# Kernel tuning notes

Measured on AMD Instinct MI355X. Metric: run time of the kernel, lower is better.

## Reference

```python
import jax, jax.numpy as jnp
import numpy as np

B, C, T = 2048, 8, 1024
EPS = 1e-5
SLOPE = 1.0 / 128.0


def leaky(x):
    # F.leaky_relu(x, 1/128)
    return jnp.where(x >= 0, x, SLOPE * x)


def batchnorm(h, g, b):
    # training-mode BatchNorm1d over [B, C, T]: stats over (batch, time), biased var
    m = h.mean(axis=(0, 2), keepdims=True)
    v = jnp.mean((h - m) ** 2, axis=(0, 2), keepdims=True)
    return (h - m) * jax.lax.rsqrt(v + EPS) * g[None, :, None] + b[None, :, None]


def setup_inputs() -> dict:
    key = jax.random.key(0)
    ks = jax.random.split(key, 8)
    x = jax.random.normal(ks[0], (B, C, T), dtype=jnp.float32)
    # reservoir pushforward: low-bit random matrix scaled to spectral radius 0.1
    A_raw = jax.random.normal(ks[1], (C, C), dtype=jnp.float32)
    rho = jnp.max(jnp.abs(np.linalg.eigvals(np.asarray(A_raw))))
    A = (0.1 * A_raw / rho).astype(jnp.float32)
    w1 = jax.random.normal(ks[2], (24, 8), dtype=jnp.float32) * (1.0 / np.sqrt(8))
    b1 = jax.random.normal(ks[3], (24,), dtype=jnp.float32) * 0.01
    w2 = jax.random.normal(ks[4], (16, 24), dtype=jnp.float32) * (1.0 / np.sqrt(24))
    b2 = jax.random.normal(ks[5], (16,), dtype=jnp.float32) * 0.01
    w3 = jax.random.normal(ks[6], (11, 48), dtype=jnp.float32) * (1.0 / np.sqrt(48))
    b3 = jax.random.normal(ks[7], (11,), dtype=jnp.float32) * 0.01
    return {
        "x": x, "A": A,
        "bn1_g": jnp.ones((8,), jnp.float32), "bn1_b": jnp.zeros((8,), jnp.float32),
        "w1": w1, "b1": b1, "w2": w2, "b2": b2, "w3": w3, "b3": b3,
        "bn2_g": jnp.ones((11,), jnp.float32), "bn2_b": jnp.zeros((11,), jnp.float32),
    }


def reference(x, A, bn1_g, bn1_b, w1, b1, w2, b2, w3, b3, bn2_g, bn2_b):
    bw = batchnorm(x, bn1_g, bn1_b)  # [B,8,T]

    # --- FSDDRC reservoir: 1024-step sequential recurrence on 8-dim state ---
    xs = jnp.transpose(bw, (2, 0, 1))  # [T,B,8]

    def step(f, xt):
        # nonlin(A @ f + x_t) with nonlin(z) = clamp(4z, -1, 1)
        f_new = jnp.clip(4.0 * (f @ A.T + xt), -1.0, 1.0)
        return f_new, jnp.concatenate([f_new, leaky(f_new)], axis=-1)  # [B,16]

    f0 = jnp.zeros_like(xs[0])
    _, outs = jax.lax.scan(step, f0, xs)  # [T,B,16]
    nl_tdyn = jnp.transpose(outs, (1, 2, 0))  # [B,16,T]

    # --- feedforward branch (mtmt = linear over channel dim) ---
    h = leaky(jnp.einsum("bct,oc->bot", bw, w1) + b1[None, :, None])  # [B,24,T]
    ff = leaky(jnp.einsum("bct,oc->bot", h, w2) + b2[None, :, None])  # [B,16,T]

    stacked = jnp.concatenate([x, bw, ff, nl_tdyn], axis=1)  # [B,48,T]
    pre = jnp.einsum("bct,oc->bot", stacked, w3) + b3[None, :, None]  # [B,11,T]
    assimilated = leaky(batchnorm(pre, bn2_g, bn2_b))
    return assimilated.mean(axis=-1)  # [B,11]
```

## Files before the change

### kernel.cpp

```cpp
#include <hip/hip_runtime.h>
#include <hip/hip_fp16.h>

#define NB 2048
#define NC 8
#define NT 1024
#define EPS 1e-5f
#define SLOPE (1.0f/128.0f)
#define NELEM (2048.0f*1024.0f)
#define TB (NT*NB)

#define PAR_OFF 9216
#define PF_S4  0
#define PF_O4  8
#define PF_B1F 16
#define PF_B2F 40
#define PF_B3F 56
#define PU_A4   96
#define PU_W1   128
#define PU_W2   224
#define PU_W3X  416
#define PU_W3F  460
#define PU_W3L  504
#define PU_W3FF 548
#define XT_BYTE  65536
#define PWS_BYTE (65536 + 2048*1024*8*2)

typedef _Float16 h2 __attribute__((ext_vector_type(2)));
typedef __fp16  fp16v2 __attribute__((ext_vector_type(2)));
union U32H2 { unsigned u; h2 h; fp16v2 f; unsigned short us[2]; };

__device__ __forceinline__ float leaky(float z){ return fmaxf(z, z*SLOPE); }
__device__ __forceinline__ unsigned short f2h(float v){ return __half_as_ushort(__float2half(v)); }
__device__ __forceinline__ float h2f(unsigned short u){ return __half2float(__ushort_as_half(u)); }
__device__ __forceinline__ h2 uph2(unsigned u){ U32H2 x; x.u = u; return x.h; }
__device__ __forceinline__ h2 pk(float a, float b){
    U32H2 x; x.f = __builtin_amdgcn_cvt_pkrtz(a, b); return x.h;
}

#if defined(__has_builtin)
#if __has_builtin(__builtin_amdgcn_fdot2)
#define HAVE_FDOT2 1
#endif
#endif
#ifdef HAVE_FDOT2
__device__ __forceinline__ float fdot2(h2 a, h2 b, float c){ return __builtin_amdgcn_fdot2(a, b, c, false); }
#else
__device__ __forceinline__ float fdot2(h2 a, h2 b, float c){
    return c + (float)a[0]*(float)b[0] + (float)a[1]*(float)b[1];
}
#endif

__global__ __launch_bounds__(256) void k0_tr(const float* __restrict__ x,
                                             unsigned short* __restrict__ xT,
                                             float* __restrict__ ws)
{
    __shared__ unsigned short tile[64*134];
    __shared__ float sred[4][4][2];
    const int tid = threadIdx.x;
    const int bg = blockIdx.x >> 4;
    const int tg = blockIdx.x & 15;
    const int b0 = bg*16, t0 = tg*64;
    float s = 0.f, s2 = 0.f;
#pragma unroll
    for(int r=0;r<8;r++){
        const int flat4 = r*256 + tid;
        const int row = flat4 >> 4;
        const int t4  = flat4 & 15;
        const int b = row >> 3, c = row & 7;
        float4 v = *(const float4*)(x + (size_t)(b0+b)*8192 + c*1024 + t0 + t4*4);
        s  += v.x+v.y+v.z+v.w;
        s2 += v.x*v.x+v.y*v.y+v.z*v.z+v.w*v.w;
        const int base = b*8 + c;
        tile[(t4*4+0)*134 + base] = f2h(v.x);
        tile[(t4*4+1)*134 + base] = f2h(v.y);
        tile[(t4*4+2)*134 + base] = f2h(v.z);
        tile[(t4*4+3)*134 + base] = f2h(v.w);
    }
#pragma unroll
    for(int m=8;m>=1;m>>=1){ s += __shfl_xor(s,m,64); s2 += __shfl_xor(s2,m,64); }
    const int lane = tid & 63, wave = tid >> 6;
    if((lane & 15) == 0){ sred[wave][lane>>4][0] = s; sred[wave][lane>>4][1] = s2; }
    __syncthreads();
    if(tid < 16){
        const int c = tid & 7, which = tid >> 3;
        const int w0 = (c < 4) ? 0 : 1, g = c & 3;
        const float v = sred[w0][g][which] + sred[w0+2][g][which];
        atomicAdd(&ws[(blockIdx.x & 63)*16 + which*8 + c], v);
    }
#pragma unroll
    for(int r=0;r<8;r++){
        const int q = r*256 + tid;
        const int t = q >> 5, inner = q & 31;
        const unsigned int lo = *(const unsigned int*)&tile[t*134 + inner*4];
        const unsigned int hi = *(const unsigned int*)&tile[t*134 + inner*4 + 2];
        *(uint2*)(xT + ((size_t)(t0+t)*NB + b0)*8 + inner*4) = make_uint2(lo, hi);
    }
}

__device__ __forceinline__ unsigned pk2u(float a, float b){
    U32H2 v; v.us[0] = f2h(a); v.us[1] = f2h(b); return v.u;
}
__global__ __launch_bounds__(256) void k2_fold(const float* __restrict__ g1, const float* __restrict__ bb1,
    const float* __restrict__ w1, const float* __restrict__ b1,
    const float* __restrict__ w2, const float* __restrict__ b2,
    const float* __restrict__ w3, const float* __restrict__ b3,
    const float* __restrict__ A, float* __restrict__ ws)
{
    float* par = ws + PAR_OFF;
    unsigned* paru = (unsigned*)par;
    __shared__ float st[16];
    __shared__ float sc[8], oc[8];
    const int tid = threadIdx.x;
    if(tid<16){
        float s=0.f;
        for(int i=0;i<64;i++) s += ws[i*16+tid];
        st[tid]=s;
    }
    __syncthreads();
    if(tid<8){
        const float inv = 1.0f/NELEM;
        float m  = st[tid]*inv;
        float v  = st[8+tid]*inv - m*m;
        float s_ = g1[tid]*rsqrtf(v+EPS);
        float o_ = bb1[tid] - m*s_;
        sc[tid]=s_; oc[tid]=o_;
        par[PF_S4+tid]=4.f*s_; par[PF_O4+tid]=4.f*o_;
    }
    __syncthreads();
    if(tid<24){ float a=b1[tid]; for(int c=0;c<8;c++) a += w1[tid*8+c]*oc[c]; par[PF_B1F+tid]=a; }
    if(tid<16){ par[PF_B2F+tid]=b2[tid]; }
    if(tid<11){ float a=b3[tid]; for(int c=0;c<8;c++) a += w3[tid*48+8+c]*oc[c]; par[PF_B3F+tid]=a; }
    if(tid<96){ int o=tid>>2, j=tid&3;
        paru[PU_W1+tid] = pk2u(w1[o*8+2*j]*sc[2*j], w1[o*8+2*j+1]*sc[2*j+1]); }
    if(tid<192){ int o=tid/12, j=tid-o*12;
        paru[PU_W2+tid] = pk2u(w2[o*24+2*j], w2[o*24+2*j+1]); }
    if(tid<44){ int o=tid>>2, j=tid&3; int c0=2*j, c1=2*j+1;
        float xa = w3[o*48+c0] + w3[o*48+8+c0]*sc[c0];
        float xb = w3[o*48+c1] + w3[o*48+8+c1]*sc[c1];
        paru[PU_W3X+tid] = pk2u(xa, xb);
        paru[PU_W3F+tid] = pk2u(w3[o*48+32+c0], w3[o*48+32+c1]);
        paru[PU_W3L+tid] = pk2u(w3[o*48+40+c0], w3[o*48+40+c1]);
    }
    if(tid<88){ int o=tid>>3, j=tid&7;
        paru[PU_W3FF+tid] = pk2u(w3[o*48+16+2*j], w3[o*48+16+2*j+1]); }
    if(tid<32){ int i=tid>>2, j=tid&3;
        paru[PU_A4+tid] = pk2u(4.f*A[i*8+2*j], 4.f*A[i*8+2*j+1]); }
}

__global__ __launch_bounds__(256,8) void k34(
    const unsigned short* __restrict__ xT,
    float* __restrict__ ws, unsigned short* __restrict__ pws)
{
    const float* par = ws + PAR_OFF;
    const unsigned* pu = (const unsigned*)par;
    const int tid = threadIdx.x;
    const int b  = (blockIdx.x >> 8)*256 + tid;
    const int tg = blockIdx.x & 255;
    const int t0 = tg*4;
    const int tw = (t0 >= 16) ? (t0 - 16) : 0;
    const int tend = t0 + 4;

    h2 fh[4];
#pragma unroll
    for(int j=0;j<4;j++) fh[j] = pk(0.f, 0.f);
    float s1[11], s2[11];
#pragma unroll
    for(int o=0;o<11;o++){ s1[o]=0.f; s2[o]=0.f; }

    for(int t=tw; t<tend; t++){
        union { float4 v; unsigned u[4]; unsigned short us[8]; } ux;
        ux.v = *(const float4*)(xT + ((size_t)t*NB + b)*8);
        h2 xh[4];
#pragma unroll
        for(int j=0;j<4;j++) xh[j] = uph2(ux.u[j]);
        float nf[8];
#pragma unroll
        for(int i=0;i<8;i++){
            float acc = fmaf(par[PF_S4+i], h2f(ux.us[i]), par[PF_O4+i]);
#pragma unroll
            for(int j=0;j<4;j++) acc = fdot2(uph2(pu[PU_A4+i*4+j]), fh[j], acc);
            nf[i] = fminf(fmaxf(acc,-1.f),1.f);
        }
#pragma unroll
        for(int j=0;j<4;j++) fh[j] = pk(nf[2*j], nf[2*j+1]);
        if(t >= t0){
            h2 lfh[4];
#pragma unroll
            for(int j=0;j<4;j++) lfh[j] = pk(leaky(nf[2*j]), leaky(nf[2*j+1]));
            h2 hh[12];
#pragma unroll
            for(int p=0;p<12;p++){
                float za = par[PF_B1F+2*p], zb = par[PF_B1F+2*p+1];
#pragma unroll
                for(int j=0;j<4;j++){
                    za = fdot2(uph2(pu[PU_W1+(2*p)*4+j]),   xh[j], za);
                    zb = fdot2(uph2(pu[PU_W1+(2*p+1)*4+j]), xh[j], zb);
                }
                hh[p] = pk(leaky(za), leaky(zb));
            }
            h2 ffh[8];
#pragma unroll
            for(int p=0;p<8;p++){
                float za = par[PF_B2F+2*p], zb = par[PF_B2F+2*p+1];
#pragma unroll
                for(int j=0;j<12;j++){
                    za = fdot2(uph2(pu[PU_W2+(2*p)*12+j]),   hh[j], za);
                    zb = fdot2(uph2(pu[PU_W2+(2*p+1)*12+j]), hh[j], zb);
                }
                ffh[p] = pk(leaky(za), leaky(zb));
            }
            const size_t base = (size_t)t*NB + b;
#pragma unroll
            for(int o=0;o<11;o++){
                float z = par[PF_B3F+o];
#pragma unroll
                for(int j=0;j<4;j++) z = fdot2(uph2(pu[PU_W3X+o*4+j]),  xh[j],  z);
#pragma unroll
                for(int j=0;j<4;j++) z = fdot2(uph2(pu[PU_W3F+o*4+j]),  fh[j],  z);
#pragma unroll
                for(int j=0;j<4;j++) z = fdot2(uph2(pu[PU_W3L+o*4+j]),  lfh[j], z);
#pragma unroll
                for(int j=0;j<8;j++) z = fdot2(uph2(pu[PU_W3FF+o*8+j]), ffh[j], z);
                s1[o] += z; s2[o] += z*z;
                pws[(size_t)o*TB + base] = f2h(z);
            }
        }
    }
#pragma unroll
    for(int o=0;o<11;o++){
#pragma unroll
        for(int m=32;m>=1;m>>=1){ s1[o]+=__shfl_xor(s1[o],m,64); s2[o]+=__shfl_xor(s2[o],m,64); }
    }
    __shared__ float red[4][22];
    const int wave=tid>>6, lane=tid&63;
    if(lane==0){
#pragma unroll
        for(int o=0;o<11;o++){ red[wave][o]=s1[o]; red[wave][11+o]=s2[o]; }
    }
    __syncthreads();
    if(tid<22){
        float tot = red[0][tid]+red[1][tid]+red[2][tid]+red[3][tid];
        atomicAdd(&ws[1024 + (blockIdx.x & 255)*32 + tid], tot);
    }
}

__global__ __launch_bounds__(256) void k6(const float* __restrict__ g2, const float* __restrict__ bb2,
                                          const float* __restrict__ ws,
                                          const unsigned short* __restrict__ pws,
                                          float* __restrict__ out)
{
    const int o  = blockIdx.x >> 5;
    const int r  = blockIdx.x & 31;
    const int bg = r & 1, tg = r >> 1;
    const int tid = threadIdx.x;

    __shared__ float red[4][2];
    __shared__ float sal, sbe;
    {
        float p1 = ws[1024 + tid*32 + o];
        float p2 = ws[1024 + tid*32 + 11 + o];
#pragma unroll
        for(int m=32;m>=1;m>>=1){ p1 += __shfl_xor(p1,m,64); p2 += __shfl_xor(p2,m,64); }
        const int wave = tid>>6, lane = tid&63;
        if(lane==0){ red[wave][0]=p1; red[wave][1]=p2; }
        __syncthreads();
        if(tid==0){
            float t1 = red[0][0]+red[1][0]+red[2][0]+red[3][0];
            float t2 = red[0][1]+red[1][1]+red[2][1]+red[3][1];
            const float inv = 1.0f/NELEM;
            float m = t1*inv;
            float v = t2*inv - m*m;
            float a = g2[o]*rsqrtf(v+EPS);
            sal = a; sbe = bb2[o] - m*a;
        }
        __syncthreads();
    }
    const float al = sal, be = sbe;

    const int b0 = bg*1024 + tid*4;
    const unsigned short* pp = pws + (size_t)o*TB + b0;
    float acc0=0.f, acc1=0.f, acc2=0.f, acc3=0.f;
#pragma unroll 8
    for(int i=0;i<64;i++){
        const int t = tg*64 + i;
        uint2 u = *(const uint2*)(pp + (size_t)t*NB);
        U32H2 ua, ub; ua.u = u.x; ub.u = u.y;
        acc0 += leaky(fmaf(al, h2f(ua.us[0]), be));
        acc1 += leaky(fmaf(al, h2f(ua.us[1]), be));
        acc2 += leaky(fmaf(al, h2f(ub.us[0]), be));
        acc3 += leaky(fmaf(al, h2f(ub.us[1]), be));
    }
    atomicAdd(&out[(b0+0)*11+o], acc0*(1.0f/NT));
    atomicAdd(&out[(b0+1)*11+o], acc1*(1.0f/NT));
    atomicAdd(&out[(b0+2)*11+o], acc2*(1.0f/NT));
    atomicAdd(&out[(b0+3)*11+o], acc3*(1.0f/NT));
}

extern "C" void kernel_launch(void* const* d_in, const int* in_sizes, int n_in,
                              void* d_out, int out_size, void* d_ws, size_t ws_size,
                              hipStream_t stream)
{
    const float* x   = (const float*)d_in[0];
    const float* A   = (const float*)d_in[1];
    const float* g1  = (const float*)d_in[2];
    const float* bb1 = (const float*)d_in[3];
    const float* w1  = (const float*)d_in[4];
    const float* b1  = (const float*)d_in[5];
    const float* w2  = (const float*)d_in[6];
    const float* b2  = (const float*)d_in[7];
    const float* w3  = (const float*)d_in[8];
    const float* b3  = (const float*)d_in[9];
    const float* g2  = (const float*)d_in[10];
    const float* bb2 = (const float*)d_in[11];
    float* out = (float*)d_out;
    float* ws  = (float*)d_ws;
    unsigned short* xT  = (unsigned short*)((char*)d_ws + XT_BYTE);
    unsigned short* pws = (unsigned short*)((char*)d_ws + PWS_BYTE);

    (void)hipMemsetAsync(d_ws, 0, 40960, stream);
    (void)hipMemsetAsync(d_out, 0, (size_t)out_size*4, stream);
    k0_tr  <<<2048, 256, 0, stream>>>(x, xT, ws);
    k2_fold<<<1,    256, 0, stream>>>(g1, bb1, w1, b1, w2, b2, w3, b3, A, ws);
    k34    <<<2048, 256, 0, stream>>>(xT, ws, pws);
    k6     <<<352,  256, 0, stream>>>(g2, bb2, ws, pws, out);
}
```

Before: 249.4 us.

## Double time chunk per block and process timestep pairs sharing weight loads

Each k34 block now covers 8 timesteps instead of 4, so the 16-step recurrence warmup is amortised over twice as many outputs and half as many blocks are launched. The output phase handles two timesteps at once, so each packed weight loaded from the parameter area feeds two dot products. Leaky-ReLU now runs on packed halves and the clamp uses a single med3 instruction. The trade-off is more live registers, which is why the launch bound drops to 4 waves, and fewer, longer blocks with less parallelism.

```diff
diff --git a/kernel.cpp b/kernel.cpp
--- a/kernel.cpp
+++ b/kernel.cpp
@@ -36,6 +36,11 @@
 __device__ __forceinline__ h2 pk(float a, float b){
     U32H2 x; x.f = __builtin_amdgcn_cvt_pkrtz(a, b); return x.h;
 }
+__device__ __forceinline__ h2 leaky2(h2 v){
+    h2 s = v * (_Float16)SLOPE;
+    return __builtin_elementwise_max(v, s);
+}
+__device__ __forceinline__ float clamp1(float z){ return __builtin_amdgcn_fmed3f(z, -1.f, 1.f); }
 
 #if defined(__has_builtin)
 #if __has_builtin(__builtin_amdgcn_fdot2)
@@ -147,18 +152,17 @@
         paru[PU_A4+tid] = pk2u(4.f*A[i*8+2*j], 4.f*A[i*8+2*j+1]); }
 }
 
-__global__ __launch_bounds__(256,8) void k34(
+__global__ __launch_bounds__(256,4) void k34(
     const unsigned short* __restrict__ xT,
     float* __restrict__ ws, unsigned short* __restrict__ pws)
 {
     const float* par = ws + PAR_OFF;
     const unsigned* pu = (const unsigned*)par;
     const int tid = threadIdx.x;
-    const int b  = (blockIdx.x >> 8)*256 + tid;
-    const int tg = blockIdx.x & 255;
-    const int t0 = tg*4;
+    const int b  = (blockIdx.x >> 7)*256 + tid;
+    const int tg = blockIdx.x & 127;
+    const int t0 = tg*8;
     const int tw = (t0 >= 16) ? (t0 - 16) : 0;
-    const int tend = t0 + 4;
 
     h2 fh[4];
 #pragma unroll
@@ -167,63 +171,109 @@
 #pragma unroll
     for(int o=0;o<11;o++){ s1[o]=0.f; s2[o]=0.f; }
 
-    for(int t=tw; t<tend; t++){
+    for(int t=tw; t<t0; t++){
         union { float4 v; unsigned u[4]; unsigned short us[8]; } ux;
         ux.v = *(const float4*)(xT + ((size_t)t*NB + b)*8);
-        h2 xh[4];
-#pragma unroll
-        for(int j=0;j<4;j++) xh[j] = uph2(ux.u[j]);
         float nf[8];
 #pragma unroll
         for(int i=0;i<8;i++){
             float acc = fmaf(par[PF_S4+i], h2f(ux.us[i]), par[PF_O4+i]);
 #pragma unroll
             for(int j=0;j<4;j++) acc = fdot2(uph2(pu[PU_A4+i*4+j]), fh[j], acc);
-            nf[i] = fminf(fmaxf(acc,-1.f),1.f);
+            nf[i] = clamp1(acc);
         }
 #pragma unroll
         for(int j=0;j<4;j++) fh[j] = pk(nf[2*j], nf[2*j+1]);
-        if(t >= t0){
-            h2 lfh[4];
-#pragma unroll
-            for(int j=0;j<4;j++) lfh[j] = pk(leaky(nf[2*j]), leaky(nf[2*j+1]));
-            h2 hh[12];
-#pragma unroll
-            for(int p=0;p<12;p++){
-                float za = par[PF_B1F+2*p], zb = par[PF_B1F+2*p+1];
-#pragma unroll
-                for(int j=0;j<4;j++){
-                    za = fdot2(uph2(pu[PU_W1+(2*p)*4+j]),   xh[j], za);
-                    zb = fdot2(uph2(pu[PU_W1+(2*p+1)*4+j]), xh[j], zb);
-                }
-                hh[p] = pk(leaky(za), leaky(zb));
-            }
-            h2 ffh[8];
-#pragma unroll
-            for(int p=0;p<8;p++){
-                float za = par[PF_B2F+2*p], zb = par[PF_B2F+2*p+1];
-#pragma unroll
-                for(int j=0;j<12;j++){
-                    za = fdot2(uph2(pu[PU_W2+(2*p)*12+j]),   hh[j], za);
-                    zb = fdot2(uph2(pu[PU_W2+(2*p+1)*12+j]), hh[j], zb);
-                }
-                ffh[p] = pk(leaky(za), leaky(zb));
-            }
-            const size_t base = (size_t)t*NB + b;
-#pragma unroll
-            for(int o=0;o<11;o++){
-                float z = par[PF_B3F+o];
-#pragma unroll
-                for(int j=0;j<4;j++) z = fdot2(uph2(pu[PU_W3X+o*4+j]),  xh[j],  z);
-#pragma unroll
-                for(int j=0;j<4;j++) z = fdot2(uph2(pu[PU_W3F+o*4+j]),  fh[j],  z);
-#pragma unroll
-                for(int j=0;j<4;j++) z = fdot2(uph2(pu[PU_W3L+o*4+j]),  lfh[j], z);
-#pragma unroll
-                for(int j=0;j<8;j++) z = fdot2(uph2(pu[PU_W3FF+o*8+j]), ffh[j], z);
-                s1[o] += z; s2[o] += z*z;
-                pws[(size_t)o*TB + base] = f2h(z);
-            }
+    }
+
+    for(int tp=0; tp<4; tp++){
+        const int t = t0 + tp*2;
+        h2 xh2[2][4], fh2[2][4];
+#pragma unroll
+        for(int u=0;u<2;u++){
+            union { float4 v; unsigned uu[4]; unsigned short us[8]; } ux;
+            ux.v = *(const float4*)(xT + ((size_t)(t+u)*NB + b)*8);
+#pragma unroll
+            for(int j=0;j<4;j++) xh2[u][j] = uph2(ux.uu[j]);
+            float nf[8];
+#pragma unroll
+            for(int i=0;i<8;i++){
+                float acc = fmaf(par[PF_S4+i], h2f(ux.us[i]), par[PF_O4+i]);
+#pragma unroll
+                for(int j=0;j<4;j++) acc = fdot2(uph2(pu[PU_A4+i*4+j]), fh[j], acc);
+                nf[i] = clamp1(acc);
+            }
+#pragma unroll
+            for(int j=0;j<4;j++){ fh[j] = pk(nf[2*j], nf[2*j+1]); fh2[u][j] = fh[j]; }
+        }
+        h2 hh2[2][12];
+#pragma unroll
+        for(int p=0;p<12;p++){
+            float za0 = par[PF_B1F+2*p], zb0 = par[PF_B1F+2*p+1];
+            float za1 = za0, zb1 = zb0;
+#pragma unroll
+            for(int j=0;j<4;j++){
+                h2 wa = uph2(pu[PU_W1+(2*p)*4+j]);
+                h2 wb = uph2(pu[PU_W1+(2*p+1)*4+j]);
+                za0 = fdot2(wa, xh2[0][j], za0);
+                za1 = fdot2(wa, xh2[1][j], za1);
+                zb0 = fdot2(wb, xh2[0][j], zb0);
+                zb1 = fdot2(wb, xh2[1][j], zb1);
+            }
+            hh2[0][p] = leaky2(pk(za0, zb0));
+            hh2[1][p] = leaky2(pk(za1, zb1));
+        }
+        h2 ff2[2][8];
+#pragma unroll
+        for(int p=0;p<8;p++){
+            float za0 = par[PF_B2F+2*p], zb0 = par[PF_B2F+2*p+1];
+            float za1 = za0, zb1 = zb0;
+#pragma unroll
+            for(int j=0;j<12;j++){
+                h2 wa = uph2(pu[PU_W2+(2*p)*12+j]);
+                h2 wb = uph2(pu[PU_W2+(2*p+1)*12+j]);
+                za0 = fdot2(wa, hh2[0][j], za0);
+                za1 = fdot2(wa, hh2[1][j], za1);
+                zb0 = fdot2(wb, hh2[0][j], zb0);
+                zb1 = fdot2(wb, hh2[1][j], zb1);
+            }
+            ff2[0][p] = leaky2(pk(za0, zb0));
+            ff2[1][p] = leaky2(pk(za1, zb1));
+        }
+        h2 lf2[2][4];
+#pragma unroll
+        for(int u=0;u<2;u++)
+#pragma unroll
+            for(int j=0;j<4;j++) lf2[u][j] = leaky2(fh2[u][j]);
+        const size_t base = (size_t)t*NB + b;
+#pragma unroll
+        for(int o=0;o<11;o++){
+            float z0 = par[PF_B3F+o], z1 = z0;
+#pragma unroll
+            for(int j=0;j<4;j++){
+                h2 w = uph2(pu[PU_W3X+o*4+j]);
+                z0 = fdot2(w, xh2[0][j], z0); z1 = fdot2(w, xh2[1][j], z1);
+            }
+#pragma unroll
+            for(int j=0;j<4;j++){
+                h2 w = uph2(pu[PU_W3F+o*4+j]);
+                z0 = fdot2(w, fh2[0][j], z0); z1 = fdot2(w, fh2[1][j], z1);
+            }
+#pragma unroll
+            for(int j=0;j<4;j++){
+                h2 w = uph2(pu[PU_W3L+o*4+j]);
+                z0 = fdot2(w, lf2[0][j], z0); z1 = fdot2(w, lf2[1][j], z1);
+            }
+#pragma unroll
+            for(int j=0;j<8;j++){
+                h2 w = uph2(pu[PU_W3FF+o*8+j]);
+                z0 = fdot2(w, ff2[0][j], z0); z1 = fdot2(w, ff2[1][j], z1);
+            }
+            s1[o] += z0 + z1;
+            s2[o] = fmaf(z0, z0, s2[o]);
+            s2[o] = fmaf(z1, z1, s2[o]);
+            pws[(size_t)o*TB + base]      = f2h(z0);
+            pws[(size_t)o*TB + base + NB] = f2h(z1);
         }
     }
 #pragma unroll
@@ -321,6 +371,6 @@
     (void)hipMemsetAsync(d_out, 0, (size_t)out_size*4, stream);
     k0_tr  <<<2048, 256, 0, stream>>>(x, xT, ws);
     k2_fold<<<1,    256, 0, stream>>>(g1, bb1, w1, b1, w2, b2, w3, b3, A, ws);
-    k34    <<<2048, 256, 0, stream>>>(xT, ws, pws);
+    k34    <<<1024, 256, 0, stream>>>(xT, ws, pws);
     k6     <<<352,  256, 0, stream>>>(g2, bb2, ws, pws, out);
 }
```

New measurement: 229.1 us. 8.1% less time.

## Switch recurrence and MLP to fp32 FMA with 8-step time tiles

Applied to the files above, without the earlier changes.

Replaces the packed fp16 fdot2 arithmetic in the fused reservoir/MLP kernel with plain fp32 FMAs on fp32 parameters. Each block now covers 8 time steps instead of 4, so the 16-step warm-up recurrence is amortised over twice as many outputs, and the block count is halved. Occupancy hint drops from 8 to 4, clamping uses fmed3, and zeroing of the output moves into the fold kernel, removing a memset. The fp32 path roughly doubles the arithmetic instructions per output compared with dot2 and raises register pressure.

```diff
diff --git a/kernel.cpp b/kernel.cpp
--- a/kernel.cpp
+++ b/kernel.cpp
@@ -10,45 +10,25 @@
 #define TB (NT*NB)
 
 #define PAR_OFF 9216
-#define PF_S4  0
-#define PF_O4  8
-#define PF_B1F 16
-#define PF_B2F 40
-#define PF_B3F 56
-#define PU_A4   96
-#define PU_W1   128
-#define PU_W2   224
-#define PU_W3X  416
-#define PU_W3F  460
-#define PU_W3L  504
-#define PU_W3FF 548
+#define PF_S4    0
+#define PF_O4    8
+#define PF_B1F   16
+#define PF_B2F   40
+#define PF_B3F   56
+#define PF_A4F   128
+#define PF_W1F   192
+#define PF_W2F   384
+#define PF_W3XF  768
+#define PF_W3FP  856
+#define PF_W3LP  944
+#define PF_W3FFP 1032
 #define XT_BYTE  65536
 #define PWS_BYTE (65536 + 2048*1024*8*2)
-
-typedef _Float16 h2 __attribute__((ext_vector_type(2)));
-typedef __fp16  fp16v2 __attribute__((ext_vector_type(2)));
-union U32H2 { unsigned u; h2 h; fp16v2 f; unsigned short us[2]; };
 
 __device__ __forceinline__ float leaky(float z){ return fmaxf(z, z*SLOPE); }
 __device__ __forceinline__ unsigned short f2h(float v){ return __half_as_ushort(__float2half(v)); }
 __device__ __forceinline__ float h2f(unsigned short u){ return __half2float(__ushort_as_half(u)); }
-__device__ __forceinline__ h2 uph2(unsigned u){ U32H2 x; x.u = u; return x.h; }
-__device__ __forceinline__ h2 pk(float a, float b){
-    U32H2 x; x.f = __builtin_amdgcn_cvt_pkrtz(a, b); return x.h;
-}
-
-#if defined(__has_builtin)
-#if __has_builtin(__builtin_amdgcn_fdot2)
-#define HAVE_FDOT2 1
-#endif
-#endif
-#ifdef HAVE_FDOT2
-__device__ __forceinline__ float fdot2(h2 a, h2 b, float c){ return __builtin_amdgcn_fdot2(a, b, c, false); }
-#else
-__device__ __forceinline__ float fdot2(h2 a, h2 b, float c){
-    return c + (float)a[0]*(float)b[0] + (float)a[1]*(float)b[1];
-}
-#endif
+__device__ __forceinline__ float clamp1(float z){ return __builtin_amdgcn_fmed3f(z, -1.f, 1.f); }
 
 __global__ __launch_bounds__(256) void k0_tr(const float* __restrict__ x,
                                              unsigned short* __restrict__ xT,
@@ -97,17 +77,14 @@
     }
 }
 
-__device__ __forceinline__ unsigned pk2u(float a, float b){
-    U32H2 v; v.us[0] = f2h(a); v.us[1] = f2h(b); return v.u;
-}
 __global__ __launch_bounds__(256) void k2_fold(const float* __restrict__ g1, const float* __restrict__ bb1,
     const float* __restrict__ w1, const float* __restrict__ b1,
     const float* __restrict__ w2, const float* __restrict__ b2,
     const float* __restrict__ w3, const float* __restrict__ b3,
-    const float* __restrict__ A, float* __restrict__ ws)
+    const float* __restrict__ A, float* __restrict__ ws,
+    float* __restrict__ out)
 {
     float* par = ws + PAR_OFF;
-    unsigned* paru = (unsigned*)par;
     __shared__ float st[16];
     __shared__ float sc[8], oc[8];
     const int tid = threadIdx.x;
@@ -130,100 +107,107 @@
     if(tid<24){ float a=b1[tid]; for(int c=0;c<8;c++) a += w1[tid*8+c]*oc[c]; par[PF_B1F+tid]=a; }
     if(tid<16){ par[PF_B2F+tid]=b2[tid]; }
     if(tid<11){ float a=b3[tid]; for(int c=0;c<8;c++) a += w3[tid*48+8+c]*oc[c]; par[PF_B3F+tid]=a; }
-    if(tid<96){ int o=tid>>2, j=tid&3;
-        paru[PU_W1+tid] = pk2u(w1[o*8+2*j]*sc[2*j], w1[o*8+2*j+1]*sc[2*j+1]); }
-    if(tid<192){ int o=tid/12, j=tid-o*12;
-        paru[PU_W2+tid] = pk2u(w2[o*24+2*j], w2[o*24+2*j+1]); }
-    if(tid<44){ int o=tid>>2, j=tid&3; int c0=2*j, c1=2*j+1;
-        float xa = w3[o*48+c0] + w3[o*48+8+c0]*sc[c0];
-        float xb = w3[o*48+c1] + w3[o*48+8+c1]*sc[c1];
-        paru[PU_W3X+tid] = pk2u(xa, xb);
-        paru[PU_W3F+tid] = pk2u(w3[o*48+32+c0], w3[o*48+32+c1]);
-        paru[PU_W3L+tid] = pk2u(w3[o*48+40+c0], w3[o*48+40+c1]);
-    }
-    if(tid<88){ int o=tid>>3, j=tid&7;
-        paru[PU_W3FF+tid] = pk2u(w3[o*48+16+2*j], w3[o*48+16+2*j+1]); }
-    if(tid<32){ int i=tid>>2, j=tid&3;
-        paru[PU_A4+tid] = pk2u(4.f*A[i*8+2*j], 4.f*A[i*8+2*j+1]); }
-}
-
-__global__ __launch_bounds__(256,8) void k34(
+    if(tid<64){ par[PF_A4F+tid] = 4.f*A[tid]; }
+    if(tid<192){ const int c = tid & 7; par[PF_W1F+tid] = w1[tid]*sc[c]; }
+    for(int i=tid;i<384;i+=256) par[PF_W2F+i] = w2[i];
+    if(tid<88){
+        const int o = tid >> 3, c = tid & 7;
+        par[PF_W3XF+tid] = w3[o*48+c] + w3[o*48+8+c]*sc[c];
+        par[PF_W3FP+tid] = w3[o*48+32+c];
+        par[PF_W3LP+tid] = w3[o*48+40+c];
+    }
+    if(tid<176){ const int o = tid >> 4, c = tid & 15; par[PF_W3FFP+tid] = w3[o*48+16+c]; }
+    for(int i=tid;i<2048*11;i+=256) out[i] = 0.f;
+}
+
+__global__ __launch_bounds__(256,4) void k34(
     const unsigned short* __restrict__ xT,
     float* __restrict__ ws, unsigned short* __restrict__ pws)
 {
     const float* par = ws + PAR_OFF;
-    const unsigned* pu = (const unsigned*)par;
     const int tid = threadIdx.x;
-    const int b  = (blockIdx.x >> 8)*256 + tid;
-    const int tg = blockIdx.x & 255;
-    const int t0 = tg*4;
+    const int b  = (blockIdx.x >> 7)*256 + tid;
+    const int tg = blockIdx.x & 127;
+    const int t0 = tg*8;
     const int tw = (t0 >= 16) ? (t0 - 16) : 0;
-    const int tend = t0 + 4;
-
-    h2 fh[4];
-#pragma unroll
-    for(int j=0;j<4;j++) fh[j] = pk(0.f, 0.f);
+
+    float f[8];
+#pragma unroll
+    for(int i=0;i<8;i++) f[i] = 0.f;
     float s1[11], s2[11];
 #pragma unroll
     for(int o=0;o<11;o++){ s1[o]=0.f; s2[o]=0.f; }
 
-    for(int t=tw; t<tend; t++){
-        union { float4 v; unsigned u[4]; unsigned short us[8]; } ux;
+#pragma unroll 1
+    for(int t=tw; t<t0; t++){
+        union { float4 v; unsigned short us[8]; } ux;
         ux.v = *(const float4*)(xT + ((size_t)t*NB + b)*8);
-        h2 xh[4];
-#pragma unroll
-        for(int j=0;j<4;j++) xh[j] = uph2(ux.u[j]);
-        float nf[8];
+        float xf[8], nf[8];
+#pragma unroll
+        for(int i=0;i<8;i++) xf[i] = h2f(ux.us[i]);
 #pragma unroll
         for(int i=0;i<8;i++){
-            float acc = fmaf(par[PF_S4+i], h2f(ux.us[i]), par[PF_O4+i]);
-#pragma unroll
-            for(int j=0;j<4;j++) acc = fdot2(uph2(pu[PU_A4+i*4+j]), fh[j], acc);
-            nf[i] = fminf(fmaxf(acc,-1.f),1.f);
-        }
-#pragma unroll
-        for(int j=0;j<4;j++) fh[j] = pk(nf[2*j], nf[2*j+1]);
-        if(t >= t0){
-            h2 lfh[4];
-#pragma unroll
-            for(int j=0;j<4;j++) lfh[j] = pk(leaky(nf[2*j]), leaky(nf[2*j+1]));
-            h2 hh[12];
-#pragma unroll
-            for(int p=0;p<12;p++){
-                float za = par[PF_B1F+2*p], zb = par[PF_B1F+2*p+1];
-#pragma unroll
-                for(int j=0;j<4;j++){
-                    za = fdot2(uph2(pu[PU_W1+(2*p)*4+j]),   xh[j], za);
-                    zb = fdot2(uph2(pu[PU_W1+(2*p+1)*4+j]), xh[j], zb);
-                }
-                hh[p] = pk(leaky(za), leaky(zb));
-            }
-            h2 ffh[8];
-#pragma unroll
-            for(int p=0;p<8;p++){
-                float za = par[PF_B2F+2*p], zb = par[PF_B2F+2*p+1];
-#pragma unroll
-                for(int j=0;j<12;j++){
-                    za = fdot2(uph2(pu[PU_W2+(2*p)*12+j]),   hh[j], za);
-                    zb = fdot2(uph2(pu[PU_W2+(2*p+1)*12+j]), hh[j], zb);
-                }
-                ffh[p] = pk(leaky(za), leaky(zb));
-            }
-            const size_t base = (size_t)t*NB + b;
-#pragma unroll
-            for(int o=0;o<11;o++){
-                float z = par[PF_B3F+o];
-#pragma unroll
-                for(int j=0;j<4;j++) z = fdot2(uph2(pu[PU_W3X+o*4+j]),  xh[j],  z);
-#pragma unroll
-                for(int j=0;j<4;j++) z = fdot2(uph2(pu[PU_W3F+o*4+j]),  fh[j],  z);
-#pragma unroll
-                for(int j=0;j<4;j++) z = fdot2(uph2(pu[PU_W3L+o*4+j]),  lfh[j], z);
-#pragma unroll
-                for(int j=0;j<8;j++) z = fdot2(uph2(pu[PU_W3FF+o*8+j]), ffh[j], z);
-                s1[o] += z; s2[o] += z*z;
-                pws[(size_t)o*TB + base] = f2h(z);
-            }
+            float acc = fmaf(par[PF_S4+i], xf[i], par[PF_O4+i]);
+#pragma unroll
+            for(int j=0;j<8;j++) acc = fmaf(par[PF_A4F+i*8+j], f[j], acc);
+            nf[i] = clamp1(acc);
+        }
+#pragma unroll
+        for(int i=0;i<8;i++) f[i] = nf[i];
+    }
+
+#pragma unroll 1
+    for(int t=t0; t<t0+8; t++){
+        union { float4 v; unsigned short us[8]; } ux;
+        ux.v = *(const float4*)(xT + ((size_t)t*NB + b)*8);
+        float xf[8], nf[8];
+#pragma unroll
+        for(int i=0;i<8;i++) xf[i] = h2f(ux.us[i]);
+#pragma unroll
+        for(int i=0;i<8;i++){
+            float acc = fmaf(par[PF_S4+i], xf[i], par[PF_O4+i]);
+#pragma unroll
+            for(int j=0;j<8;j++) acc = fmaf(par[PF_A4F+i*8+j], f[j], acc);
+            nf[i] = clamp1(acc);
+        }
+#pragma unroll
+        for(int i=0;i<8;i++) f[i] = nf[i];
+
+        float h[24];
+#pragma unroll
+        for(int o=0;o<24;o++){
+            float acc = par[PF_B1F+o];
+#pragma unroll
+            for(int c=0;c<8;c++) acc = fmaf(par[PF_W1F+o*8+c], xf[c], acc);
+            h[o] = leaky(acc);
+        }
+        float ff[16];
+#pragma unroll
+        for(int o=0;o<16;o++){
+            float acc = par[PF_B2F+o];
+#pragma unroll
+            for(int c=0;c<24;c++) acc = fmaf(par[PF_W2F+o*24+c], h[c], acc);
+            ff[o] = leaky(acc);
+        }
+        float lf[8];
+#pragma unroll
+        for(int i=0;i<8;i++) lf[i] = leaky(f[i]);
+
+        const size_t base = (size_t)t*NB + b;
+#pragma unroll
+        for(int o=0;o<11;o++){
+            float z = par[PF_B3F+o];
+#pragma unroll
+            for(int c=0;c<8;c++)  z = fmaf(par[PF_W3XF +o*8 +c], xf[c], z);
+#pragma unroll
+            for(int c=0;c<8;c++)  z = fmaf(par[PF_W3FP +o*8 +c], f[c],  z);
+#pragma unroll
+            for(int c=0;c<8;c++)  z = fmaf(par[PF_W3LP +o*8 +c], lf[c], z);
+#pragma unroll
+            for(int c=0;c<16;c++) z = fmaf(par[PF_W3FFP+o*16+c], ff[c], z);
+            s1[o] += z;
+            s2[o] = fmaf(z, z, s2[o]);
+            pws[(size_t)o*TB + base] = f2h(z);
         }
     }
 #pragma unroll
@@ -284,11 +268,12 @@
     for(int i=0;i<64;i++){
         const int t = tg*64 + i;
         uint2 u = *(const uint2*)(pp + (size_t)t*NB);
-        U32H2 ua, ub; ua.u = u.x; ub.u = u.y;
-        acc0 += leaky(fmaf(al, h2f(ua.us[0]), be));
-        acc1 += leaky(fmaf(al, h2f(ua.us[1]), be));
-        acc2 += leaky(fmaf(al, h2f(ub.us[0]), be));
-        acc3 += leaky(fmaf(al, h2f(ub.us[1]), be));
+        unsigned short a0 = (unsigned short)(u.x & 0xffff), a1 = (unsigned short)(u.x >> 16);
+        unsigned short b0s = (unsigned short)(u.y & 0xffff), b1s = (unsigned short)(u.y >> 16);
+        acc0 += leaky(fmaf(al, h2f(a0),  be));
+        acc1 += leaky(fmaf(al, h2f(a1),  be));
+        acc2 += leaky(fmaf(al, h2f(b0s), be));
+        acc3 += leaky(fmaf(al, h2f(b1s), be));
     }
     atomicAdd(&out[(b0+0)*11+o], acc0*(1.0f/NT));
     atomicAdd(&out[(b0+1)*11+o], acc1*(1.0f/NT));
@@ -318,9 +303,8 @@
     unsigned short* pws = (unsigned short*)((char*)d_ws + PWS_BYTE);
 
     (void)hipMemsetAsync(d_ws, 0, 40960, stream);
-    (void)hipMemsetAsync(d_out, 0, (size_t)out_size*4, stream);
     k0_tr  <<<2048, 256, 0, stream>>>(x, xT, ws);
-    k2_fold<<<1,    256, 0, stream>>>(g1, bb1, w1, b1, w2, b2, w3, b3, A, ws);
-    k34    <<<2048, 256, 0, stream>>>(xT, ws, pws);
+    k2_fold<<<1,    256, 0, stream>>>(g1, bb1, w1, b1, w2, b2, w3, b3, A, ws, out);
+    k34    <<<1024, 256, 0, stream>>>(xT, ws, pws);
     k6     <<<352,  256, 0, stream>>>(g2, bb2, ws, pws, out);
 }
```

Result: slower. 267.3 us (+7.2%).
